# Kernel optimization log

Measured on AMD Instinct MI355X. Metric: run time of the kernel, lower is better.

## Reference

```python
import jax, jax.numpy as jnp
import numpy as np
import math

RADIUS = 1.0
RES = 128
S = 1024                      # marching steps per ray (target_step_size)
N = 16384                     # rays
STEP = RADIUS * 2.0 * math.sqrt(3.0) / S   # render_step_size
T_EPS = 1e-4                  # nerfacc early-termination transmittance threshold


def setup_inputs() -> dict:
    key = jax.random.key(0)
    k1, k2, k3, k4, k5, k6 = jax.random.split(key, 6)
    rays_o = jax.random.uniform(k1, (N, 3), jnp.float32, -0.5, 0.5)
    rays_d = jax.random.normal(k2, (N, 3), jnp.float32)
    rays_d = rays_d / jnp.linalg.norm(rays_d, axis=-1, keepdims=True)
    jitter = jax.random.uniform(k3, (N,), jnp.float32)          # stratified per-ray offset
    binaries = jax.random.uniform(k4, (RES * RES * RES,)) < 0.3
    Wd = jax.random.normal(k5, (3, 1), jnp.float32) * 0.5        # density_query params
    bd = jax.random.normal(k6, (1,), jnp.float32) * 0.1 + 1.0
    return {"rays_o": rays_o, "rays_d": rays_d, "jitter": jitter,
            "Wd": Wd, "bd": bd, "binaries": binaries}


def _march(rays_o, rays_d, jitter, Wd, bd, binaries):
    r = RADIUS
    inv_d = 1.0 / rays_d
    t0 = (-r - rays_o) * inv_d
    t1 = (r - rays_o) * inv_d
    t_near = jnp.maximum(jnp.max(jnp.minimum(t0, t1), axis=-1), 0.0)   # [N]
    t_far = jnp.min(jnp.maximum(t0, t1), axis=-1)                       # [N]
    hit = t_near < t_far

    # stratified uniform marching: t_i = t_near + (i + jitter) * step
    i = jnp.arange(S, dtype=jnp.float32)
    t_starts = t_near[:, None] + (i[None, :] + jitter[:, None]) * STEP  # [N,S]
    t_ends = t_starts + STEP
    mid = (t_starts + t_ends) * 0.5
    pts = rays_o[:, None, :] + rays_d[:, None, :] * mid[..., None]      # [N,S,3]

    # occupancy-grid lookup (irregular gather)
    idx = jnp.clip(jnp.floor((pts + r) / (2.0 * r) * RES), 0, RES - 1).astype(jnp.int32)
    flat = (idx[..., 0] * RES + idx[..., 1]) * RES + idx[..., 2]        # [N,S]
    occ = binaries[flat]
    in_box = (t_ends < t_far[:, None]) & hit[:, None]
    valid = occ & in_box

    # density query at sample midpoints (sigma_fn), zeroed on skipped cells
    sigma = jax.nn.relu(pts @ Wd + bd)[..., 0] * valid                  # [N,S]

    # transmittance before each sample; early-terminate when T <= 1e-4
    tau = jnp.cumsum(sigma * STEP, axis=-1)
    T = jnp.exp(-(tau - sigma * STEP))
    keep = valid & (T > T_EPS)
    return t_starts, t_ends, sigma, keep


def reference(rays_o, rays_d, jitter, Wd, bd, binaries):
    t_starts, t_ends, sigma, keep = _march(rays_o, rays_d, jitter, Wd, bd, binaries)
    keep_f = keep.astype(t_starts.dtype)
    # padded/masked equivalent of nerfacc's ragged (ray_indices, t_starts, t_ends)
    ray_indices = jnp.broadcast_to(jnp.arange(N, dtype=jnp.int32)[:, None], (N, S))
    return ray_indices, t_starts * keep_f, t_ends * keep_f, keep
```

## Files before the change

### kernel.cpp

```cpp
#include <hip/hip_runtime.h>

#define NRAYS 16384
#define SSTEPS 1024
#define GRES 128
#define NSAMP ((size_t)NRAYS * (size_t)SSTEPS)

extern "C" __global__ __launch_bounds__(256) void NeRFAccSampler_55791625175295_kernel(
    const float* __restrict__ rays_o,
    const float* __restrict__ rays_d,
    const float* __restrict__ jitter,
    const float* __restrict__ Wd,
    const float* __restrict__ bd,
    const unsigned char* __restrict__ binaries,
    float* __restrict__ out)
{
#pragma clang fp contract(off)
    const int tid  = blockIdx.x * 256 + (int)threadIdx.x;
    const int ray  = tid >> 6;
    const int lane = (int)threadIdx.x & 63;
    if (ray >= NRAYS) return;

    const float STEP = (float)(2.0 * 1.7320508075688772 / 1024.0);
    const float KEEP_THR = 9.2103405f;

    const float ox = rays_o[3 * ray + 0], oy = rays_o[3 * ray + 1], oz = rays_o[3 * ray + 2];
    const float dx = rays_d[3 * ray + 0], dy = rays_d[3 * ray + 1], dz = rays_d[3 * ray + 2];
    const float jit = jitter[ray];
    const float w0 = Wd[0], w1 = Wd[1], w2 = Wd[2], bb = bd[0];

    const float ivx = 1.0f / dx, ivy = 1.0f / dy, ivz = 1.0f / dz;
    const float t0x = (-1.0f - ox) * ivx;
    const float t1x = ( 1.0f - ox) * ivx;
    const float t0y = (-1.0f - oy) * ivy;
    const float t1y = ( 1.0f - oy) * ivy;
    const float t0z = (-1.0f - oz) * ivz;
    const float t1z = ( 1.0f - oz) * ivz;
    const float tnx = t0x < t1x ? t0x : t1x, tXx = t0x > t1x ? t0x : t1x;
    const float tny = t0y < t1y ? t0y : t1y, tXy = t0y > t1y ? t0y : t1y;
    const float tnz = t0z < t1z ? t0z : t1z, tXz = t0z > t1z ? t0z : t1z;
    float t_near = tnx;
    if (tny > t_near) t_near = tny;
    if (tnz > t_near) t_near = tnz;
    if (t_near < 0.0f) t_near = 0.0f;
    float t_far = tXx;
    if (tXy < t_far) t_far = tXy;
    if (tXz < t_far) t_far = tXz;
    const bool hit = t_near < t_far;

    const size_t base  = (size_t)ray * (size_t)SSTEPS;
    const float  ray_f = (float)ray;
    const float4 o0v   = make_float4(ray_f, ray_f, ray_f, ray_f);

    float tau = 0.0f;

    for (int it = 0; it < 4; ++it) {
        const int s0 = (it << 8) + (lane << 2);

        float ts[4], te[4], loc[4];
        bool  vld[4];
        float sum = 0.0f;

        #pragma unroll
        for (int k = 0; k < 4; ++k) {
            const float fi = (float)(s0 + k);
            const float t_start = t_near + (fi + jit) * STEP;
            const float t_end   = t_start + STEP;
            const float mid     = (t_start + t_end) * 0.5f;
            const float px = ox + dx * mid;
            const float py = oy + dy * mid;
            const float pz = oz + dz * mid;

            float vx = (px + 1.0f) * 64.0f;
            float vy = (py + 1.0f) * 64.0f;
            float vz = (pz + 1.0f) * 64.0f;
            if (!(vx > 0.0f)) vx = 0.0f;
            if (vx > 127.0f)  vx = 127.0f;
            if (!(vy > 0.0f)) vy = 0.0f;
            if (vy > 127.0f)  vy = 127.0f;
            if (!(vz > 0.0f)) vz = 0.0f;
            if (vz > 127.0f)  vz = 127.0f;
            const int flat = (((int)vx * GRES) + (int)vy) * GRES + (int)vz;
            const bool occ = binaries[flat] != 0;

            const bool valid = occ && (t_end < t_far) && hit;

            float sig = ((px * w0 + py * w1) + pz * w2) + bb;
            if (sig < 0.0f) sig = 0.0f;
            const float sstep = (valid ? sig : 0.0f) * STEP;

            ts[k]  = t_start;
            te[k]  = t_end;
            vld[k] = valid;
            loc[k] = sum;
            sum    = sum + sstep;
        }

        float run = sum;
        #pragma unroll
        for (int d = 1; d < 64; d <<= 1) {
            const float y = __shfl_up(run, d, 64);
            if (lane >= d) run += y;
        }
        const float exbase = tau + (run - sum);
        tau += __shfl(run, 63, 64);

        float o1[4], o2[4], o3[4];
        #pragma unroll
        for (int k = 0; k < 4; ++k) {
            const float excl = exbase + loc[k];
            const bool keep  = vld[k] && (excl < KEEP_THR);
            o1[k] = keep ? ts[k] : 0.0f;
            o2[k] = keep ? te[k] : 0.0f;
            o3[k] = keep ? 1.0f  : 0.0f;
        }

        const size_t o = base + (size_t)s0;
        *reinterpret_cast<float4*>(&out[o])             = o0v;
        *reinterpret_cast<float4*>(&out[NSAMP + o])     = make_float4(o1[0], o1[1], o1[2], o1[3]);
        *reinterpret_cast<float4*>(&out[2 * NSAMP + o]) = make_float4(o2[0], o2[1], o2[2], o2[3]);
        *reinterpret_cast<float4*>(&out[3 * NSAMP + o]) = make_float4(o3[0], o3[1], o3[2], o3[3]);
    }
}

extern "C" void kernel_launch(void* const* d_in, const int* in_sizes, int n_in,
                              void* d_out, int out_size, void* d_ws, size_t ws_size,
                              hipStream_t stream) {
    const float* rays_o           = (const float*)d_in[0];
    const float* rays_d           = (const float*)d_in[1];
    const float* jitter           = (const float*)d_in[2];
    const float* Wd               = (const float*)d_in[3];
    const float* bd               = (const float*)d_in[4];
    const unsigned char* binaries = (const unsigned char*)d_in[5];
    float* out                    = (float*)d_out;

    NeRFAccSampler_55791625175295_kernel<<<NRAYS / 4, 256, 0, stream>>>(
        rays_o, rays_d, jitter, Wd, bd, binaries, out);
}
```

Baseline: 49.77 us.

## Process 16 contiguous samples per lane with a single wavefront scan

Each lane now handles 16 consecutive samples of its ray instead of four chunks of 4 samples, so the transmittance prefix sum needs only one 64-lane shuffle scan rather than four. Validity bits are packed into a bitmask to save registers. All 16 occupancy gathers can be issued before the scan, increasing memory-level parallelism. In exchange, each store instruction writes lane-strided 16-byte pieces rather than fully contiguous runs, which may hurt write coalescing, and register pressure rises.

Result: slower. 92.27 us (+85.4%).

```diff
diff --git a/kernel.cpp b/kernel.cpp
--- a/kernel.cpp
+++ b/kernel.cpp
@@ -47,78 +47,78 @@
     if (tXz < t_far) t_far = tXz;
     const bool hit = t_near < t_far;
 
-    const size_t base  = (size_t)ray * (size_t)SSTEPS;
+    const int   s0 = lane << 4;
+    const float t_lane0 = t_near + jit * STEP;
+
+    float loc[16];
+    unsigned int vmask = 0;
+    float sum = 0.0f;
+
+    #pragma unroll
+    for (int k = 0; k < 16; ++k) {
+        const float fi = (float)(s0 + k);
+        const float t_start = t_near + (fi + jit) * STEP;
+        const float t_end   = t_start + STEP;
+        const float mid     = (t_start + t_end) * 0.5f;
+        const float px = ox + dx * mid;
+        const float py = oy + dy * mid;
+        const float pz = oz + dz * mid;
+
+        float vx = (px + 1.0f) * 64.0f;
+        float vy = (py + 1.0f) * 64.0f;
+        float vz = (pz + 1.0f) * 64.0f;
+        if (!(vx > 0.0f)) vx = 0.0f;
+        if (vx > 127.0f)  vx = 127.0f;
+        if (!(vy > 0.0f)) vy = 0.0f;
+        if (vy > 127.0f)  vy = 127.0f;
+        if (!(vz > 0.0f)) vz = 0.0f;
+        if (vz > 127.0f)  vz = 127.0f;
+        const int flat = (((int)vx * GRES) + (int)vy) * GRES + (int)vz;
+        const bool occ = binaries[flat] != 0;
+
+        const bool valid = occ && (t_end < t_far) && hit;
+
+        float sig = ((px * w0 + py * w1) + pz * w2) + bb;
+        if (sig < 0.0f) sig = 0.0f;
+        const float sstep = (valid ? sig : 0.0f) * STEP;
+
+        vmask |= (valid ? 1u : 0u) << k;
+        loc[k] = sum;
+        sum    = sum + sstep;
+    }
+
+    float run = sum;
+    #pragma unroll
+    for (int d = 1; d < 64; d <<= 1) {
+        const float y = __shfl_up(run, d, 64);
+        if (lane >= d) run += y;
+    }
+    const float exbase = run - sum;
+
+    const size_t base  = (size_t)ray * (size_t)SSTEPS + (size_t)s0;
     const float  ray_f = (float)ray;
     const float4 o0v   = make_float4(ray_f, ray_f, ray_f, ray_f);
 
-    float tau = 0.0f;
-
-    for (int it = 0; it < 4; ++it) {
-        const int s0 = (it << 8) + (lane << 2);
-
-        float ts[4], te[4], loc[4];
-        bool  vld[4];
-        float sum = 0.0f;
-
+    #pragma unroll
+    for (int g = 0; g < 4; ++g) {
+        float a1[4], a2[4], a3[4];
         #pragma unroll
-        for (int k = 0; k < 4; ++k) {
-            const float fi = (float)(s0 + k);
-            const float t_start = t_near + (fi + jit) * STEP;
-            const float t_end   = t_start + STEP;
-            const float mid     = (t_start + t_end) * 0.5f;
-            const float px = ox + dx * mid;
-            const float py = oy + dy * mid;
-            const float pz = oz + dz * mid;
-
-            float vx = (px + 1.0f) * 64.0f;
-            float vy = (py + 1.0f) * 64.0f;
-            float vz = (pz + 1.0f) * 64.0f;
-            if (!(vx > 0.0f)) vx = 0.0f;
-            if (vx > 127.0f)  vx = 127.0f;
-            if (!(vy > 0.0f)) vy = 0.0f;
-            if (vy > 127.0f)  vy = 127.0f;
-            if (!(vz > 0.0f)) vz = 0.0f;
-            if (vz > 127.0f)  vz = 127.0f;
-            const int flat = (((int)vx * GRES) + (int)vy) * GRES + (int)vz;
-            const bool occ = binaries[flat] != 0;
-
-            const bool valid = occ && (t_end < t_far) && hit;
-
-            float sig = ((px * w0 + py * w1) + pz * w2) + bb;
-            if (sig < 0.0f) sig = 0.0f;
-            const float sstep = (valid ? sig : 0.0f) * STEP;
-
-            ts[k]  = t_start;
-            te[k]  = t_end;
-            vld[k] = valid;
-            loc[k] = sum;
-            sum    = sum + sstep;
+        for (int j = 0; j < 4; ++j) {
+            const int   k       = (g << 2) + j;
+            const float t_start = t_lane0 + (float)(s0 + k) * STEP;
+            const float ts = t_near + ((float)(s0 + k) + jit) * STEP;
+            const float te = ts + STEP;
+            const bool keep = ((vmask >> k) & 1u) && ((exbase + loc[k]) < KEEP_THR);
+            a1[j] = keep ? ts : 0.0f;
+            a2[j] = keep ? te : 0.0f;
+            a3[j] = keep ? 1.0f : 0.0f;
+            (void)t_start;
         }
-
-        float run = sum;
-        #pragma unroll
-        for (int d = 1; d < 64; d <<= 1) {
-            const float y = __shfl_up(run, d, 64);
-            if (lane >= d) run += y;
-        }
-        const float exbase = tau + (run - sum);
-        tau += __shfl(run, 63, 64);
-
-        float o1[4], o2[4], o3[4];
-        #pragma unroll
-        for (int k = 0; k < 4; ++k) {
-            const float excl = exbase + loc[k];
-            const bool keep  = vld[k] && (excl < KEEP_THR);
-            o1[k] = keep ? ts[k] : 0.0f;
-            o2[k] = keep ? te[k] : 0.0f;
-            o3[k] = keep ? 1.0f  : 0.0f;
-        }
-
-        const size_t o = base + (size_t)s0;
+        const size_t o = base + (size_t)(g << 2);
         *reinterpret_cast<float4*>(&out[o])             = o0v;
-        *reinterpret_cast<float4*>(&out[NSAMP + o])     = make_float4(o1[0], o1[1], o1[2], o1[3]);
-        *reinterpret_cast<float4*>(&out[2 * NSAMP + o]) = make_float4(o2[0], o2[1], o2[2], o2[3]);
-        *reinterpret_cast<float4*>(&out[3 * NSAMP + o]) = make_float4(o3[0], o3[1], o3[2], o3[3]);
+        *reinterpret_cast<float4*>(&out[NSAMP + o])     = make_float4(a1[0], a1[1], a1[2], a1[3]);
+        *reinterpret_cast<float4*>(&out[2 * NSAMP + o]) = make_float4(a2[0], a2[1], a2[2], a2[3]);
+        *reinterpret_cast<float4*>(&out[3 * NSAMP + o]) = make_float4(a3[0], a3[1], a3[2], a3[3]);
     }
 }
 
```
